# Optimization experiments

Hardware: AMD Instinct MI355X
Metric: run time of the kernel (lower is better)

The kernel has to match this reference:

```python
import jax, jax.numpy as jnp
import numpy as np

NUM_ATOMS = 100000
NUM_BONDS = 200000
MAX_NB = 6
ATOM_FDIM = 133
BOND_FDIM = 147
HIDDEN = 300
READOUT = 512
DEPTH = 6
ATOMS_PER_MOL = 25
NUM_MOLS = NUM_ATOMS // ATOMS_PER_MOL


def setup_inputs() -> dict:
    key = jax.random.key(0)
    ks = jax.random.split(key, 16)
    s = 0.02
    inp = {
        "f_atoms": jax.random.normal(ks[0], (NUM_ATOMS, ATOM_FDIM), jnp.float32),
        "f_bonds": jax.random.normal(ks[1], (NUM_BONDS, BOND_FDIM), jnp.float32),
        "a2b": jax.random.randint(ks[2], (NUM_ATOMS, MAX_NB), 0, NUM_BONDS),
        "b2a": jax.random.randint(ks[3], (NUM_BONDS,), 0, NUM_ATOMS),
        "b2revb": jax.random.randint(ks[4], (NUM_BONDS,), 0, NUM_BONDS),
        "mol_id": jnp.arange(NUM_ATOMS) // ATOMS_PER_MOL,
        # parameters (Linear: y = x @ W + b)
        "W_i": jax.random.normal(ks[5], (BOND_FDIM, HIDDEN), jnp.float32) * s,
        "b_i": jnp.zeros((HIDDEN,), jnp.float32),
        "W_h": jax.random.normal(ks[6], (HIDDEN, HIDDEN), jnp.float32) * s,
        "b_h": jnp.zeros((HIDDEN,), jnp.float32),
        "W_o": jax.random.normal(ks[7], (ATOM_FDIM + HIDDEN, HIDDEN), jnp.float32) * s,
        "b_o": jnp.zeros((HIDDEN,), jnp.float32),
        "W_fc0": jax.random.normal(ks[8], (HIDDEN, READOUT), jnp.float32) * s,
        "b_fc0": jnp.zeros((READOUT,), jnp.float32),
        "W_fc1": jax.random.normal(ks[9], (READOUT, READOUT), jnp.float32) * s,
        "b_fc1": jnp.zeros((READOUT,), jnp.float32),
        "W_last": jax.random.normal(ks[10], (READOUT, 1), jnp.float32) * s,
        "b_last": jnp.zeros((1,), jnp.float32),
    }
    return inp


def reference(f_atoms, f_bonds, W_i, b_i, W_h, b_h, W_o, b_o,
              W_fc0, b_fc0, W_fc1, b_fc1, W_last, b_last,
              a2b, b2a, b2revb, mol_id):
    relu = jax.nn.relu
    # input = W_i(f_bonds); message = relu(input)  (dropout p=0 -> identity)
    inp = f_bonds @ W_i + b_i                      # [B, H]
    message = relu(inp)
    for _ in range(DEPTH - 1):
        nei = message[a2b]                          # [A, nb, H] gather
        a_message = nei.sum(axis=1)                 # [A, H]
        rev_message = message[b2revb]               # [B, H]
        message = a_message[b2a] - rev_message      # [B, H]
        message = relu(inp + (message @ W_h + b_h))
    # final atom aggregation
    a_message = message[a2b].sum(axis=1)            # [A, H]
    a_input = jnp.concatenate([f_atoms, a_message], axis=1)
    atom_hiddens = relu(a_input @ W_o + b_o)        # [A, H]
    # molecule mean-pool (a_scope -> segment mean over mol_id)
    sums = jax.ops.segment_sum(atom_hiddens, mol_id, num_segments=NUM_MOLS)
    counts = jax.ops.segment_sum(jnp.ones((atom_hiddens.shape[0], 1), atom_hiddens.dtype),
                                 mol_id, num_segments=NUM_MOLS)
    mol_vecs = sums / jnp.maximum(counts, 1.0)      # [M, H]
    # readout MLP
    h = relu(mol_vecs @ W_fc0 + b_fc0)
    h = relu(h @ W_fc1 + b_fc1)
    out = h @ W_last + b_last                       # [M, 1]
    return out.reshape(-1)
```

## Files before the change

### kernel.cpp

```cpp
#include <hip/hip_runtime.h>

#define NATOMS 100000
#define NBONDS 200000
#define NMOLS  4000

typedef __bf16 bf16x8 __attribute__((ext_vector_type(8)));
typedef float  f32x4  __attribute__((ext_vector_type(4)));

__device__ unsigned short g_packWi [5  * 40 * 512];
__device__ unsigned short g_packWh [10 * 40 * 512];
__device__ unsigned short g_packWoT[5  * 40 * 512];
__device__ unsigned short g_packWoB[10 * 40 * 512];

__device__ __forceinline__ float bf2f(unsigned short u) {
    union { unsigned int i; float f; } c; c.i = ((unsigned int)u) << 16; return c.f;
}
__device__ __forceinline__ unsigned short f2bf(float f) {
    union { float f; unsigned int i; } c; c.f = f;
    unsigned int r = (c.i + 0x7FFFu + ((c.i >> 16) & 1u)) >> 16;
    return (unsigned short)r;
}
__device__ __forceinline__ unsigned int relu2(unsigned int u) {
    if (u & 0x00008000u) u &= 0xFFFF0000u;
    if (u & 0x80000000u) u &= 0x0000FFFFu;
    return u;
}

__global__ void pack_weights(const float* __restrict__ W_i,
                             const float* __restrict__ W_h,
                             const float* __restrict__ W_o)
{
    const int gid = blockIdx.x * blockDim.x + threadIdx.x;
    if (gid >= 1200 * 512) return;
    const int gg = gid >> 9;
    const int t  = gid & 511;
    const float* src; int K; unsigned short* dst; int lg;
    if (gg < 200)      { lg = gg;       src = W_i;             K = 147; dst = g_packWi; }
    else if (gg < 600) { lg = gg - 200; src = W_h;             K = 300; dst = g_packWh; }
    else if (gg < 800) { lg = gg - 600; src = W_o;             K = 133; dst = g_packWoT; }
    else               { lg = gg - 800; src = W_o + 133 * 300; K = 300; dst = g_packWoB; }
    const int s  = lg / 40, r = lg % 40;
    const int nh = r / 20, fr = (r % 20) >> 1, hl = r & 1;
    const int ln = t >> 3, j = t & 7;
    const int k = 32 * s + 8 * (ln >> 4) + j;
    const int n = 16 * (nh * 10 + fr) + (ln & 15);
    float val = (k < K && n < 300) ? src[k * 300 + n] : 0.f;
    unsigned short hi = f2bf(val);
    dst[(long)lg * 512 + t] = hl ? f2bf(val - bf2f(hi)) : hi;
}

__global__ __launch_bounds__(512, 4)
void gemm_mfma5(const void* __restrict__ Ap, int a16, int sel,
                const float* __restrict__ bias, const float* __restrict__ Cin,
                void* __restrict__ outR, int r16,
                unsigned short* __restrict__ outP16,
                long M, int K, int ksteps, int do_relu)
{
    __shared__ unsigned long long lds8[57344 / 8];
    unsigned short* Asm0 = (unsigned short*)lds8;
    unsigned short* Bsm  = (unsigned short*)lds8 + 8192;
    unsigned short* ep   = (unsigned short*)lds8;

    const unsigned short* pp =
        (sel == 0) ? g_packWi : (sel == 1) ? g_packWh :
        (sel == 2) ? g_packWoT : g_packWoB;

    const int tid = threadIdx.x;
    const int wv  = tid >> 6;
    const int ln  = tid & 63;
    const int l15 = ln & 15;
    const int g   = ln >> 4;
    const int wm  = wv >> 1;
    const int wn  = wv & 1;
    const long row0 = (long)blockIdx.x * 128;

    f32x4 acc[2][10];
#pragma unroll
    for (int m = 0; m < 2; ++m)
#pragma unroll
        for (int f = 0; f < 10; ++f) acc[m][f] = (f32x4){0.f, 0.f, 0.f, 0.f};

    int aoff[2];
#pragma unroll
    for (int m = 0; m < 2; ++m) {
        const int r = wm * 32 + m * 16 + l15;
        aoff[m] = r * 32 + 8 * (g ^ ((r >> 1) & 3));
    }

    const int srow = tid >> 2, sq = tid & 3;
    const int sqs  = sq ^ ((srow >> 1) & 3);

#define STAGE_A(BUF, SS)                                                       \
    do {                                                                       \
        if (a16) {                                                             \
            const char* src = (const char*)Ap +                                \
                (row0 + srow) * (size_t)600 + (SS) * 64 + sqs * 16;            \
            char* dst = (char*)Asm0 + (BUF) * 8192 + srow * 64 + sq * 16;      \
            __builtin_amdgcn_global_load_lds(                                  \
                (const __attribute__((address_space(1))) void*)src,            \
                (__attribute__((address_space(3))) void*)dst, 16, 0, 0);       \
        } else {                                                               \
            const float* A = (const float*)Ap;                                 \
            const long gr = row0 + srow;                                       \
            const int kb = (SS) * 32 + sqs * 8;                                \
            unsigned short tv[8];                                              \
            _Pragma("unroll")                                                  \
            for (int e = 0; e < 8; ++e)                                        \
                tv[e] = (gr < M && kb + e < K) ? f2bf(A[gr * (long)K + kb + e]) \
                                               : (unsigned short)0;            \
            ushort4 w0 = {tv[0], tv[1], tv[2], tv[3]};                         \
            ushort4 w1 = {tv[4], tv[5], tv[6], tv[7]};                         \
            *(ushort4*)(Asm0 + (BUF) * 4096 + srow * 32 + sq * 8)     = w0;    \
            *(ushort4*)(Asm0 + (BUF) * 4096 + srow * 32 + sq * 8 + 4) = w1;    \
        }                                                                      \
    } while (0)

#define STAGE_B(SS)                                                            \
    do {                                                                       \
        _Pragma("unroll")                                                      \
        for (int i = 0; i < 5; ++i) {                                          \
            const char* src = (const char*)pp + (size_t)(SS) * 40960           \
                              + i * 8192 + tid * 16;                           \
            char* dst = (char*)Bsm + i * 8192 + tid * 16;                      \
            __builtin_amdgcn_global_load_lds(                                  \
                (const __attribute__((address_space(1))) void*)src,            \
                (__attribute__((address_space(3))) void*)dst, 16, 0, 0);       \
        }                                                                      \
    } while (0)

    STAGE_A(0, 0);
    for (int s = 0; s < ksteps; ++s) {
        STAGE_B(s);
        if (s + 1 < ksteps) STAGE_A((s + 1) & 1, s + 1);
        __syncthreads();
        const unsigned short* Ab = Asm0 + (s & 1) * 4096;
        bf16x8 av[2];
#pragma unroll
        for (int m = 0; m < 2; ++m) av[m] = *(const bf16x8*)(Ab + aoff[m]);
#pragma unroll
        for (int f = 0; f < 10; ++f) {
            const int ch = wn * 20 + f * 2;
            bf16x8 bh = *(const bf16x8*)(Bsm + (ch + 0) * 512 + ln * 8);
            bf16x8 bl = *(const bf16x8*)(Bsm + (ch + 1) * 512 + ln * 8);
#pragma unroll
            for (int m = 0; m < 2; ++m) {
                acc[m][f] = __builtin_amdgcn_mfma_f32_16x16x32_bf16(av[m], bh, acc[m][f], 0, 0, 0);
                acc[m][f] = __builtin_amdgcn_mfma_f32_16x16x32_bf16(av[m], bl, acc[m][f], 0, 0, 0);
            }
        }
        __syncthreads();
    }
#undef STAGE_A
#undef STAGE_B

    if (r16) {
        for (int p = 0; p < 2; ++p) {
            if (p) __syncthreads();
            if ((wm >> 1) == p) {
                const int rbase = (wm & 1) * 32;
#pragma unroll
                for (int f = 0; f < 10; ++f) {
                    const int n = (wn * 10 + f) * 16 + l15;
                    if (n >= 300) continue;
                    const float bv = bias ? bias[n] : 0.f;
#pragma unroll
                    for (int m = 0; m < 2; ++m)
#pragma unroll
                        for (int rr = 0; rr < 4; ++rr) {
                            const int rl = rbase + m * 16 + g * 4 + rr;
                            ep[rl * 304 + n] = f2bf(acc[m][f][rr] + bv);
                        }
                }
            }
            __syncthreads();
            for (int c = tid; c < 4800; c += 512) {
                const int row = c / 75, off = c - row * 75;
                const long grow = row0 + p * 64 + row;
                if (grow >= M) continue;
                uint2 v = *(const uint2*)(ep + row * 304 + off * 4);
                if (outP16)
                    *(uint2*)(outP16 + grow * 300 + off * 4) = v;
                if (do_relu) { v.x = relu2(v.x); v.y = relu2(v.y); }
                *(uint2*)((unsigned short*)outR + grow * 300 + off * 4) = v;
            }
        }
    } else {
#pragma unroll
        for (int f = 0; f < 10; ++f) {
            const int n = (wn * 10 + f) * 16 + l15;
            if (n >= 300) continue;
            const float bv = bias ? bias[n] : 0.f;
#pragma unroll
            for (int m = 0; m < 2; ++m) {
#pragma unroll
                for (int rr = 0; rr < 4; ++rr) {
                    const long row = row0 + wm * 32 + m * 16 + g * 4 + rr;
                    if (row >= M) continue;
                    float v = acc[m][f][rr] + bv;
                    if (Cin) v += Cin[row * 300 + n];
                    if (do_relu) v = fmaxf(v, 0.f);
                    ((float*)outR)[row * 300 + n] = v;
                }
            }
        }
    }
}

__global__ __launch_bounds__(256)
void gemm_flex(const float* __restrict__ A,
               const float* __restrict__ W,
               const float* __restrict__ bias,
               float* __restrict__ outR,
               int M, int K, int N, int do_relu)
{
    __shared__ float As[16][132];
    __shared__ float Bs[16][132];

    const int tid  = threadIdx.x;
    const int tx   = tid & 15;
    const int ty   = tid >> 4;
    const int row0 = blockIdx.y * 128;
    const int col0 = blockIdx.x * 128;

    float acc[8][8];
#pragma unroll
    for (int i = 0; i < 8; ++i)
#pragma unroll
        for (int j = 0; j < 8; ++j) acc[i][j] = 0.f;

    for (int k0 = 0; k0 < K; k0 += 16) {
        {
            const int c  = tid & 15;
            const int rb = tid >> 4;
#pragma unroll
            for (int i = 0; i < 8; ++i) {
                const int r  = rb + (i << 4);
                const int gr = row0 + r, gc = k0 + c;
                As[c][r] = (gr < M && gc < K) ? A[(long)gr * K + gc] : 0.f;
            }
        }
        {
            const int c  = tid & 127;
            const int rb = tid >> 7;
#pragma unroll
            for (int i = 0; i < 8; ++i) {
                const int r  = rb + (i << 1);
                const int gr = k0 + r, gc = col0 + c;
                Bs[r][c] = (gr < K && gc < N) ? W[(long)gr * N + gc] : 0.f;
            }
        }
        __syncthreads();
#pragma unroll
        for (int kk = 0; kk < 16; ++kk) {
            const float4* As4 = reinterpret_cast<const float4*>(&As[kk][0]);
            const float4* Bs4 = reinterpret_cast<const float4*>(&Bs[kk][0]);
            float4 a0 = As4[ty], a1 = As4[ty + 16];
            float4 b0 = Bs4[tx], b1 = Bs4[tx + 16];
            float av[8] = {a0.x, a0.y, a0.z, a0.w, a1.x, a1.y, a1.z, a1.w};
            float bv[8] = {b0.x, b0.y, b0.z, b0.w, b1.x, b1.y, b1.z, b1.w};
#pragma unroll
            for (int i = 0; i < 8; ++i)
#pragma unroll
                for (int j = 0; j < 8; ++j)
                    acc[i][j] = fmaf(av[i], bv[j], acc[i][j]);
        }
        __syncthreads();
    }
#pragma unroll
    for (int i = 0; i < 8; ++i) {
        const int lr = (i < 4) ? (ty * 4 + i) : (64 + ty * 4 + (i - 4));
        const int gr = row0 + lr;
        if (gr >= M) continue;
#pragma unroll
        for (int j = 0; j < 8; ++j) {
            const int lc = (j < 4) ? (tx * 4 + j) : (64 + tx * 4 + (j - 4));
            const int gc = col0 + lc;
            if (gc >= N) continue;
            float v = acc[i][j];
            if (bias) v += bias[gc];
            if (do_relu) v = fmaxf(v, 0.f);
            outR[(long)gr * N + gc] = v;
        }
    }
}

__global__ void aggregate_bf16(const unsigned short* __restrict__ src,
                               const int* __restrict__ a2b,
                               unsigned short* __restrict__ dst)
{
    const int idx = blockIdx.x * blockDim.x + threadIdx.x;
    if (idx >= NATOMS * 75) return;
    const int a = idx / 75;
    const int q = idx - a * 75;
    const int* nb = a2b + a * 6;
    float s0 = 0.f, s1 = 0.f, s2 = 0.f, s3 = 0.f;
#pragma unroll
    for (int k = 0; k < 6; ++k) {
        const ushort4 v = *reinterpret_cast<const ushort4*>(src + (long)nb[k] * 300 + (q << 2));
        s0 += bf2f(v.x); s1 += bf2f(v.y); s2 += bf2f(v.z); s3 += bf2f(v.w);
    }
    ushort4 r;
    r.x = f2bf(s0); r.y = f2bf(s1); r.z = f2bf(s2); r.w = f2bf(s3);
    *reinterpret_cast<ushort4*>(dst + ((long)idx << 2)) = r;
}

__global__ void fused_update(const unsigned short* __restrict__ t,
                             const int* __restrict__ a2b,
                             const int* __restrict__ b2a,
                             const int* __restrict__ b2revb,
                             const float* __restrict__ b_h,
                             const unsigned short* __restrict__ inp,
                             unsigned short* __restrict__ dst)
{
    const int idx = blockIdx.x * blockDim.x + threadIdx.x;
    if (idx >= NBONDS * 75) return;
    const int b = idx / 75;
    const int q = idx - b * 75;
    const long own = (long)b * 300 + (q << 2);
    const ushort4 vi = *reinterpret_cast<const ushort4*>(inp + own);
    const float4 vh = *reinterpret_cast<const float4*>(b_h + (q << 2));
    float s0 = bf2f(vi.x) + vh.x;
    float s1 = bf2f(vi.y) + vh.y;
    float s2 = bf2f(vi.z) + vh.z;
    float s3 = bf2f(vi.w) + vh.w;
    const int a = b2a[b];
    const int* nb = a2b + a * 6;
#pragma unroll
    for (int k = 0; k < 6; ++k) {
        const ushort4 v = *reinterpret_cast<const ushort4*>(t + (long)nb[k] * 300 + (q << 2));
        s0 += bf2f(v.x); s1 += bf2f(v.y); s2 += bf2f(v.z); s3 += bf2f(v.w);
    }
    {
        const ushort4 v = *reinterpret_cast<const ushort4*>(t + (long)b2revb[b] * 300 + (q << 2));
        s0 -= bf2f(v.x); s1 -= bf2f(v.y); s2 -= bf2f(v.z); s3 -= bf2f(v.w);
    }
    ushort4 o;
    o.x = f2bf(fmaxf(s0, 0.f));
    o.y = f2bf(fmaxf(s1, 0.f));
    o.z = f2bf(fmaxf(s2, 0.f));
    o.w = f2bf(fmaxf(s3, 0.f));
    *reinterpret_cast<ushort4*>(dst + own) = o;
}

__global__ void pool_kernel(const float* __restrict__ ah, float* __restrict__ mol)
{
    const int idx = blockIdx.x * blockDim.x + threadIdx.x;
    if (idx >= NMOLS * 75) return;
    const int m = idx / 75;
    const int q = idx - m * 75;
    const float* base = ah + (long)m * 25 * 300 + (q << 2);
    float s0 = 0.f, s1 = 0.f, s2 = 0.f, s3 = 0.f;
#pragma unroll
    for (int a = 0; a < 25; ++a) {
        const float4 v = *reinterpret_cast<const float4*>(base + a * 300);
        s0 += v.x; s1 += v.y; s2 += v.z; s3 += v.w;
    }
    float4 r; r.x = s0 / 25.f; r.y = s1 / 25.f; r.z = s2 / 25.f; r.w = s3 / 25.f;
    *reinterpret_cast<float4*>(mol + ((long)idx << 2)) = r;
}

__global__ void diag_kernel(float* __restrict__ out, float wsmb)
{
    const int i = blockIdx.x * blockDim.x + threadIdx.x;
    if (i < NMOLS) out[i] = (i == 0) ? wsmb : 0.f;
}

extern "C" void kernel_launch(void* const* d_in, const int* in_sizes, int n_in,
                              void* d_out, int out_size, void* d_ws, size_t ws_size,
                              hipStream_t stream)
{
    const float* f_atoms = (const float*)d_in[0];
    const float* f_bonds = (const float*)d_in[1];
    const int*   a2b     = (const int*)d_in[2];
    const int*   b2a     = (const int*)d_in[3];
    const int*   b2revb  = (const int*)d_in[4];
    const float* W_i    = (const float*)d_in[6];
    const float* b_i    = (const float*)d_in[7];
    const float* W_h    = (const float*)d_in[8];
    const float* b_h    = (const float*)d_in[9];
    const float* W_o    = (const float*)d_in[10];
    const float* b_o    = (const float*)d_in[11];
    const float* W_fc0  = (const float*)d_in[12];
    const float* b_fc0  = (const float*)d_in[13];
    const float* W_fc1  = (const float*)d_in[14];
    const float* b_fc1  = (const float*)d_in[15];
    const float* W_last = (const float*)d_in[16];
    const float* b_last = (const float*)d_in[17];
    float* out = (float*)d_out;

    if (ws_size < 240000000ull) {
        diag_kernel<<<(NMOLS + 255) / 256, 256, 0, stream>>>(out, (float)(ws_size >> 20));
        return;
    }

    const int gBond = (NBONDS + 127) / 128;
    const int gAtom = (NATOMS + 127) / 128;
    const int aggBlocks = (NATOMS * 75 + 255) / 256;
    const int updBlocks = (NBONDS * 75 + 255) / 256;

    pack_weights<<<(1200 * 512 + 255) / 256, 256, 0, stream>>>(W_i, W_h, W_o);

    if (ws_size >= 360000000ull) {
        unsigned short* inpB = (unsigned short*)d_ws;
        unsigned short* msgB = (unsigned short*)((char*)d_ws + 120000000);
        unsigned short* tB   = (unsigned short*)((char*)d_ws + 240000000);
        unsigned short* amB  = (unsigned short*)d_ws;
        float* tmpF = (float*)((char*)d_ws + 120000000);
        float* molF = (float*)((char*)d_ws + 240000000);
        float* h0   = molF + 2000000;
        float* h1   = molF + 5000000;

        gemm_mfma5<<<gBond, 512, 0, stream>>>(f_bonds, 0, 0, b_i, nullptr,
                                              msgB, 1, inpB, NBONDS, 147, 5, 1);
        for (int d = 0; d < 5; ++d) {
            gemm_mfma5<<<gBond, 512, 0, stream>>>(msgB, 1, 1, nullptr, nullptr,
                                                  tB, 1, nullptr, NBONDS, 300, 10, 0);
            fused_update<<<updBlocks, 256, 0, stream>>>(tB, a2b, b2a, b2revb, b_h,
                                                        inpB, msgB);
        }
        aggregate_bf16<<<aggBlocks, 256, 0, stream>>>(msgB, a2b, amB);
        gemm_mfma5<<<gAtom, 512, 0, stream>>>(f_atoms, 0, 2, nullptr, nullptr,
                                              tmpF, 0, nullptr, NATOMS, 133, 5, 0);
        gemm_mfma5<<<gAtom, 512, 0, stream>>>(amB, 1, 3, b_o, tmpF,
                                              tmpF, 0, nullptr, NATOMS, 300, 10, 1);
        pool_kernel<<<(NMOLS * 75 + 255) / 256, 256, 0, stream>>>(tmpF, molF);
        gemm_flex<<<dim3(4, 32), 256, 0, stream>>>(molF, W_fc0, b_fc0, h0, NMOLS, 300, 512, 1);
        gemm_flex<<<dim3(4, 32), 256, 0, stream>>>(h0, W_fc1, b_fc1, h1, NMOLS, 512, 512, 1);
        gemm_flex<<<dim3(1, 32), 256, 0, stream>>>(h1, W_last, b_last, out, NMOLS, 512, 1, 0);
    } else {
        unsigned short* msgB = (unsigned short*)d_ws;
        unsigned short* tB   = (unsigned short*)((char*)d_ws + 120000000);
        unsigned short* amB  = tB;
        float* tmpF = (float*)d_ws;
        float* molF = (float*)((char*)d_ws + 180000000);
        float* h0   = molF + 2000000;
        float* h1   = molF + 5000000;

        gemm_mfma5<<<gBond, 512, 0, stream>>>(f_bonds, 0, 0, b_i, nullptr,
                                              msgB, 1, nullptr, NBONDS, 147, 5, 1);
        for (int d = 0; d < 5; ++d) {
            gemm_mfma5<<<gBond, 512, 0, stream>>>(msgB, 1, 1, nullptr, nullptr,
                                                  tB, 1, nullptr, NBONDS, 300, 10, 0);
            gemm_mfma5<<<gBond, 512, 0, stream>>>(f_bonds, 0, 0, b_i, nullptr,
                                                  msgB, 1, nullptr, NBONDS, 147, 5, 0);
            fused_update<<<updBlocks, 256, 0, stream>>>(tB, a2b, b2a, b2revb, b_h,
                                                        msgB, msgB);
        }
        aggregate_bf16<<<aggBlocks, 256, 0, stream>>>(msgB, a2b, amB);
        gemm_mfma5<<<gAtom, 512, 0, stream>>>(f_atoms, 0, 2, nullptr, nullptr,
                                              tmpF, 0, nullptr, NATOMS, 133, 5, 0);
        gemm_mfma5<<<gAtom, 512, 0, stream>>>(amB, 1, 3, b_o, tmpF,
                                              tmpF, 0, nullptr, NATOMS, 300, 10, 1);
        pool_kernel<<<(NMOLS * 75 + 255) / 256, 256, 0, stream>>>(tmpF, molF);
        gemm_flex<<<dim3(4, 32), 256, 0, stream>>>(molF, W_fc0, b_fc0, h0, NMOLS, 300, 512, 1);
        gemm_flex<<<dim3(4, 32), 256, 0, stream>>>(h0, W_fc1, b_fc1, h1, NMOLS, 512, 512, 1);
        gemm_flex<<<dim3(1, 32), 256, 0, stream>>>(h1, W_last, b_last, out, NMOLS, 512, 1, 0);
    }
}
```

Baseline: 2.317 ms.

## Double-buffer B weight tiles and remap waves to 2x4 grid in MFMA GEMM

The GEMM kernel now double-buffers the packed weight (B) tiles in LDS alongside A, so the next k-step's A and B loads are issued before computing the current one, leaving one barrier per step instead of two. The wave layout changes from 4x2 to 2x4, with each wave covering 64 rows by 5 column fragments, which raises A-fragment reuse per B load. The weight packing is simplified to a linear fragment order to match. LDS use grows to 96KB per block, which may limit blocks per CU and lower occupancy.

```diff
diff --git a/kernel.cpp b/kernel.cpp
--- a/kernel.cpp
+++ b/kernel.cpp
@@ -39,27 +39,27 @@
     else if (gg < 600) { lg = gg - 200; src = W_h;             K = 300; dst = g_packWh; }
     else if (gg < 800) { lg = gg - 600; src = W_o;             K = 133; dst = g_packWoT; }
     else               { lg = gg - 800; src = W_o + 133 * 300; K = 300; dst = g_packWoB; }
-    const int s  = lg / 40, r = lg % 40;
-    const int nh = r / 20, fr = (r % 20) >> 1, hl = r & 1;
+    const int s = lg / 40, r = lg % 40;
+    const int f = r >> 1, hl = r & 1;
     const int ln = t >> 3, j = t & 7;
     const int k = 32 * s + 8 * (ln >> 4) + j;
-    const int n = 16 * (nh * 10 + fr) + (ln & 15);
+    const int n = 16 * f + (ln & 15);
     float val = (k < K && n < 300) ? src[k * 300 + n] : 0.f;
     unsigned short hi = f2bf(val);
     dst[(long)lg * 512 + t] = hl ? f2bf(val - bf2f(hi)) : hi;
 }
 
-__global__ __launch_bounds__(512, 4)
-void gemm_mfma5(const void* __restrict__ Ap, int a16, int sel,
+__global__ __launch_bounds__(512)
+void gemm_mfma6(const void* __restrict__ Ap, int a16, int sel,
                 const float* __restrict__ bias, const float* __restrict__ Cin,
                 void* __restrict__ outR, int r16,
                 unsigned short* __restrict__ outP16,
                 long M, int K, int ksteps, int do_relu)
 {
-    __shared__ unsigned long long lds8[57344 / 8];
-    unsigned short* Asm0 = (unsigned short*)lds8;
-    unsigned short* Bsm  = (unsigned short*)lds8 + 8192;
-    unsigned short* ep   = (unsigned short*)lds8;
+    __shared__ unsigned long long lds8[98304 / 8];
+    unsigned short* Asm = (unsigned short*)lds8;
+    unsigned short* Bsm = (unsigned short*)lds8 + 8192;
+    unsigned short* ep  = (unsigned short*)lds8;
 
     const unsigned short* pp =
         (sel == 0) ? g_packWi : (sel == 1) ? g_packWh :
@@ -70,20 +70,20 @@
     const int ln  = tid & 63;
     const int l15 = ln & 15;
     const int g   = ln >> 4;
-    const int wm  = wv >> 1;
-    const int wn  = wv & 1;
+    const int wm  = wv >> 2;
+    const int wn  = wv & 3;
     const long row0 = (long)blockIdx.x * 128;
 
-    f32x4 acc[2][10];
-#pragma unroll
-    for (int m = 0; m < 2; ++m)
-#pragma unroll
-        for (int f = 0; f < 10; ++f) acc[m][f] = (f32x4){0.f, 0.f, 0.f, 0.f};
-
-    int aoff[2];
-#pragma unroll
-    for (int m = 0; m < 2; ++m) {
-        const int r = wm * 32 + m * 16 + l15;
+    f32x4 acc[4][5];
+#pragma unroll
+    for (int m = 0; m < 4; ++m)
+#pragma unroll
+        for (int f = 0; f < 5; ++f) acc[m][f] = (f32x4){0.f, 0.f, 0.f, 0.f};
+
+    int aoff[4];
+#pragma unroll
+    for (int m = 0; m < 4; ++m) {
+        const int r = wm * 64 + m * 16 + l15;
         aoff[m] = r * 32 + 8 * (g ^ ((r >> 1) & 3));
     }
 
@@ -95,7 +95,7 @@
         if (a16) {                                                             \
             const char* src = (const char*)Ap +                                \
                 (row0 + srow) * (size_t)600 + (SS) * 64 + sqs * 16;            \
-            char* dst = (char*)Asm0 + (BUF) * 8192 + srow * 64 + sq * 16;      \
+            char* dst = (char*)Asm + (BUF) * 8192 + srow * 64 + sq * 16;       \
             __builtin_amdgcn_global_load_lds(                                  \
                 (const __attribute__((address_space(1))) void*)src,            \
                 (__attribute__((address_space(3))) void*)dst, 16, 0, 0);       \
@@ -110,18 +110,18 @@
                                                : (unsigned short)0;            \
             ushort4 w0 = {tv[0], tv[1], tv[2], tv[3]};                         \
             ushort4 w1 = {tv[4], tv[5], tv[6], tv[7]};                         \
-            *(ushort4*)(Asm0 + (BUF) * 4096 + srow * 32 + sq * 8)     = w0;    \
-            *(ushort4*)(Asm0 + (BUF) * 4096 + srow * 32 + sq * 8 + 4) = w1;    \
+            *(ushort4*)(Asm + (BUF) * 4096 + srow * 32 + sq * 8)     = w0;     \
+            *(ushort4*)(Asm + (BUF) * 4096 + srow * 32 + sq * 8 + 4) = w1;     \
         }                                                                      \
     } while (0)
 
-#define STAGE_B(SS)                                                            \
+#define STAGE_B(BUF, SS)                                                       \
     do {                                                                       \
         _Pragma("unroll")                                                      \
         for (int i = 0; i < 5; ++i) {                                          \
             const char* src = (const char*)pp + (size_t)(SS) * 40960           \
                               + i * 8192 + tid * 16;                           \
-            char* dst = (char*)Bsm + i * 8192 + tid * 16;                      \
+            char* dst = (char*)Bsm + (BUF) * 40960 + i * 8192 + tid * 16;      \
             __builtin_amdgcn_global_load_lds(                                  \
                 (const __attribute__((address_space(1))) void*)src,            \
                 (__attribute__((address_space(3))) void*)dst, 16, 0, 0);       \
@@ -129,24 +129,30 @@
     } while (0)
 
     STAGE_A(0, 0);
+    STAGE_B(0, 0);
+    __syncthreads();
     for (int s = 0; s < ksteps; ++s) {
-        STAGE_B(s);
-        if (s + 1 < ksteps) STAGE_A((s + 1) & 1, s + 1);
-        __syncthreads();
-        const unsigned short* Ab = Asm0 + (s & 1) * 4096;
-        bf16x8 av[2];
-#pragma unroll
-        for (int m = 0; m < 2; ++m) av[m] = *(const bf16x8*)(Ab + aoff[m]);
-#pragma unroll
-        for (int f = 0; f < 10; ++f) {
-            const int ch = wn * 20 + f * 2;
-            bf16x8 bh = *(const bf16x8*)(Bsm + (ch + 0) * 512 + ln * 8);
-            bf16x8 bl = *(const bf16x8*)(Bsm + (ch + 1) * 512 + ln * 8);
-#pragma unroll
-            for (int m = 0; m < 2; ++m) {
+        const int cur = s & 1;
+        if (s + 1 < ksteps) {
+            STAGE_A(cur ^ 1, s + 1);
+            STAGE_B(cur ^ 1, s + 1);
+        }
+        const unsigned short* Ab = Asm + cur * 4096;
+        const unsigned short* Bb = Bsm + cur * 20480;
+        bf16x8 av[4];
+#pragma unroll
+        for (int m = 0; m < 4; ++m) av[m] = *(const bf16x8*)(Ab + aoff[m]);
+#pragma unroll
+        for (int f = 0; f < 5; ++f) {
+            const int fg = wn * 5 + f;
+            bf16x8 bh = *(const bf16x8*)(Bb + (2 * fg + 0) * 512 + ln * 8);
+            bf16x8 bl = *(const bf16x8*)(Bb + (2 * fg + 1) * 512 + ln * 8);
+#pragma unroll
+            for (int m = 0; m < 4; ++m)
                 acc[m][f] = __builtin_amdgcn_mfma_f32_16x16x32_bf16(av[m], bh, acc[m][f], 0, 0, 0);
+#pragma unroll
+            for (int m = 0; m < 4; ++m)
                 acc[m][f] = __builtin_amdgcn_mfma_f32_16x16x32_bf16(av[m], bl, acc[m][f], 0, 0, 0);
-            }
         }
         __syncthreads();
     }
@@ -156,18 +162,17 @@
     if (r16) {
         for (int p = 0; p < 2; ++p) {
             if (p) __syncthreads();
-            if ((wm >> 1) == p) {
-                const int rbase = (wm & 1) * 32;
-#pragma unroll
-                for (int f = 0; f < 10; ++f) {
-                    const int n = (wn * 10 + f) * 16 + l15;
+            if (wm == p) {
+#pragma unroll
+                for (int f = 0; f < 5; ++f) {
+                    const int n = (wn * 5 + f) * 16 + l15;
                     if (n >= 300) continue;
                     const float bv = bias ? bias[n] : 0.f;
 #pragma unroll
-                    for (int m = 0; m < 2; ++m)
+                    for (int m = 0; m < 4; ++m)
 #pragma unroll
                         for (int rr = 0; rr < 4; ++rr) {
-                            const int rl = rbase + m * 16 + g * 4 + rr;
+                            const int rl = m * 16 + g * 4 + rr;
                             ep[rl * 304 + n] = f2bf(acc[m][f][rr] + bv);
                         }
                 }
@@ -186,15 +191,15 @@
         }
     } else {
 #pragma unroll
-        for (int f = 0; f < 10; ++f) {
-            const int n = (wn * 10 + f) * 16 + l15;
+        for (int f = 0; f < 5; ++f) {
+            const int n = (wn * 5 + f) * 16 + l15;
             if (n >= 300) continue;
             const float bv = bias ? bias[n] : 0.f;
 #pragma unroll
-            for (int m = 0; m < 2; ++m) {
+            for (int m = 0; m < 4; ++m) {
 #pragma unroll
                 for (int rr = 0; rr < 4; ++rr) {
-                    const long row = row0 + wm * 32 + m * 16 + g * 4 + rr;
+                    const long row = row0 + wm * 64 + m * 16 + g * 4 + rr;
                     if (row >= M) continue;
                     float v = acc[m][f][rr] + bv;
                     if (Cin) v += Cin[row * 300 + n];
@@ -410,18 +415,18 @@
         float* h0   = molF + 2000000;
         float* h1   = molF + 5000000;
 
-        gemm_mfma5<<<gBond, 512, 0, stream>>>(f_bonds, 0, 0, b_i, nullptr,
+        gemm_mfma6<<<gBond, 512, 0, stream>>>(f_bonds, 0, 0, b_i, nullptr,
                                               msgB, 1, inpB, NBONDS, 147, 5, 1);
         for (int d = 0; d < 5; ++d) {
-            gemm_mfma5<<<gBond, 512, 0, stream>>>(msgB, 1, 1, nullptr, nullptr,
+            gemm_mfma6<<<gBond, 512, 0, stream>>>(msgB, 1, 1, nullptr, nullptr,
                                                   tB, 1, nullptr, NBONDS, 300, 10, 0);
             fused_update<<<updBlocks, 256, 0, stream>>>(tB, a2b, b2a, b2revb, b_h,
                                                         inpB, msgB);
         }
         aggregate_bf16<<<aggBlocks, 256, 0, stream>>>(msgB, a2b, amB);
-        gemm_mfma5<<<gAtom, 512, 0, stream>>>(f_atoms, 0, 2, nullptr, nullptr,
+        gemm_mfma6<<<gAtom, 512, 0, stream>>>(f_atoms, 0, 2, nullptr, nullptr,
                                               tmpF, 0, nullptr, NATOMS, 133, 5, 0);
-        gemm_mfma5<<<gAtom, 512, 0, stream>>>(amB, 1, 3, b_o, tmpF,
+        gemm_mfma6<<<gAtom, 512, 0, stream>>>(amB, 1, 3, b_o, tmpF,
                                               tmpF, 0, nullptr, NATOMS, 300, 10, 1);
         pool_kernel<<<(NMOLS * 75 + 255) / 256, 256, 0, stream>>>(tmpF, molF);
         gemm_flex<<<dim3(4, 32), 256, 0, stream>>>(molF, W_fc0, b_fc0, h0, NMOLS, 300, 512, 1);
@@ -436,20 +441,20 @@
         float* h0   = molF + 2000000;
         float* h1   = molF + 5000000;
 
-        gemm_mfma5<<<gBond, 512, 0, stream>>>(f_bonds, 0, 0, b_i, nullptr,
+        gemm_mfma6<<<gBond, 512, 0, stream>>>(f_bonds, 0, 0, b_i, nullptr,
                                               msgB, 1, nullptr, NBONDS, 147, 5, 1);
         for (int d = 0; d < 5; ++d) {
-            gemm_mfma5<<<gBond, 512, 0, stream>>>(msgB, 1, 1, nullptr, nullptr,
+            gemm_mfma6<<<gBond, 512, 0, stream>>>(msgB, 1, 1, nullptr, nullptr,
                                                   tB, 1, nullptr, NBONDS, 300, 10, 0);
-            gemm_mfma5<<<gBond, 512, 0, stream>>>(f_bonds, 0, 0, b_i, nullptr,
+            gemm_mfma6<<<gBond, 512, 0, stream>>>(f_bonds, 0, 0, b_i, nullptr,
                                                   msgB, 1, nullptr, NBONDS, 147, 5, 0);
             fused_update<<<updBlocks, 256, 0, stream>>>(tB, a2b, b2a, b2revb, b_h,
                                                         msgB, msgB);
         }
         aggregate_bf16<<<aggBlocks, 256, 0, stream>>>(msgB, a2b, amB);
-        gemm_mfma5<<<gAtom, 512, 0, stream>>>(f_atoms, 0, 2, nullptr, nullptr,
+        gemm_mfma6<<<gAtom, 512, 0, stream>>>(f_atoms, 0, 2, nullptr, nullptr,
                                               tmpF, 0, nullptr, NATOMS, 133, 5, 0);
-        gemm_mfma5<<<gAtom, 512, 0, stream>>>(amB, 1, 3, b_o, tmpF,
+        gemm_mfma6<<<gAtom, 512, 0, stream>>>(amB, 1, 3, b_o, tmpF,
                                               tmpF, 0, nullptr, NATOMS, 300, 10, 1);
         pool_kernel<<<(NMOLS * 75 + 255) / 256, 256, 0, stream>>>(tmpF, molF);
         gemm_flex<<<dim3(4, 32), 256, 0, stream>>>(molF, W_fc0, b_fc0, h0, NMOLS, 300, 512, 1);
```

Result: slower. 2.537 ms (+9.5%).

## Fuse message gather into W_h GEMM A-loading and fuse update epilogue

Applied to the files above, without the earlier changes.

The message-passing step now gathers the neighbour messages (six a2b neighbours of the source atom minus the reverse bond) inside the GEMM's A-tile staging, and applies the input residual, bias and ReLU in the GEMM epilogue. This removes the separate fused_update kernel and the intermediate tB round-trip per depth, and uses ping-pong message buffers. Weight packing is simplified to a linear column-fragment order. In exchange, the GEMM A-staging becomes seven scattered row loads per tile and per k-step instead of asynchronous direct-to-LDS loads. The per-bond gather is also recomputed for every k-step, and the recomputed sum is rounded to bf16 before the matmul.

```diff
diff --git a/kernel.cpp b/kernel.cpp
--- a/kernel.cpp
+++ b/kernel.cpp
@@ -39,27 +39,32 @@
     else if (gg < 600) { lg = gg - 200; src = W_h;             K = 300; dst = g_packWh; }
     else if (gg < 800) { lg = gg - 600; src = W_o;             K = 133; dst = g_packWoT; }
     else               { lg = gg - 800; src = W_o + 133 * 300; K = 300; dst = g_packWoB; }
-    const int s  = lg / 40, r = lg % 40;
-    const int nh = r / 20, fr = (r % 20) >> 1, hl = r & 1;
+    const int s = lg / 40, r = lg % 40;
+    const int f = r >> 1, hl = r & 1;
     const int ln = t >> 3, j = t & 7;
     const int k = 32 * s + 8 * (ln >> 4) + j;
-    const int n = 16 * (nh * 10 + fr) + (ln & 15);
+    const int n = 16 * f + (ln & 15);
     float val = (k < K && n < 300) ? src[k * 300 + n] : 0.f;
     unsigned short hi = f2bf(val);
     dst[(long)lg * 512 + t] = hl ? f2bf(val - bf2f(hi)) : hi;
 }
 
 __global__ __launch_bounds__(512, 4)
-void gemm_mfma5(const void* __restrict__ Ap, int a16, int sel,
-                const float* __restrict__ bias, const float* __restrict__ Cin,
+void gemm_mfma8(const void* __restrict__ Ap, int mode, int sel,
+                const float* __restrict__ bias,
+                const float* __restrict__ cinF,
+                const unsigned short* __restrict__ cin16,
                 void* __restrict__ outR, int r16,
                 unsigned short* __restrict__ outP16,
+                const int* __restrict__ b2a,
+                const int* __restrict__ a2b,
+                const int* __restrict__ b2revb,
                 long M, int K, int ksteps, int do_relu)
 {
     __shared__ unsigned long long lds8[57344 / 8];
-    unsigned short* Asm0 = (unsigned short*)lds8;
-    unsigned short* Bsm  = (unsigned short*)lds8 + 8192;
-    unsigned short* ep   = (unsigned short*)lds8;
+    unsigned short* Asm = (unsigned short*)lds8;
+    unsigned short* Bsm = (unsigned short*)lds8 + 8192;
+    unsigned short* ep  = (unsigned short*)lds8;
 
     const unsigned short* pp =
         (sel == 0) ? g_packWi : (sel == 1) ? g_packWh :
@@ -90,15 +95,56 @@
     const int srow = tid >> 2, sq = tid & 3;
     const int sqs  = sq ^ ((srow >> 1) & 3);
 
+    int gnb0 = 0, gnb1 = 0, gnb2 = 0, gnb3 = 0, gnb4 = 0, gnb5 = 0, grev = 0;
+    bool gok = false;
+    if (mode == 2) {
+        const long brow = row0 + srow;
+        gok = (brow < M);
+        const int bi = gok ? (int)brow : 0;
+        const int a  = b2a[bi];
+        grev = b2revb[bi];
+        const int* nb = a2b + a * 6;
+        gnb0 = nb[0]; gnb1 = nb[1]; gnb2 = nb[2];
+        gnb3 = nb[3]; gnb4 = nb[4]; gnb5 = nb[5];
+    }
+
+#define GROW(idx, sgn)                                                         \
+    do {                                                                       \
+        const unsigned short* rp = (const unsigned short*)Ap +                 \
+            (long)(idx) * 300 + kb;                                            \
+        const uint2 u0 = *(const uint2*)(rp);                                  \
+        const uint2 u1 = *(const uint2*)(rp + 4);                              \
+        s0 sgn bf2f((unsigned short)(u0.x & 0xFFFF));                          \
+        s1 sgn bf2f((unsigned short)(u0.x >> 16));                             \
+        s2 sgn bf2f((unsigned short)(u0.y & 0xFFFF));                          \
+        s3 sgn bf2f((unsigned short)(u0.y >> 16));                             \
+        s4 sgn bf2f((unsigned short)(u1.x & 0xFFFF));                          \
+        s5 sgn bf2f((unsigned short)(u1.x >> 16));                             \
+        s6 sgn bf2f((unsigned short)(u1.y & 0xFFFF));                          \
+        s7 sgn bf2f((unsigned short)(u1.y >> 16));                             \
+    } while (0)
+
 #define STAGE_A(BUF, SS)                                                       \
     do {                                                                       \
-        if (a16) {                                                             \
+        if (mode == 1) {                                                       \
             const char* src = (const char*)Ap +                                \
                 (row0 + srow) * (size_t)600 + (SS) * 64 + sqs * 16;            \
-            char* dst = (char*)Asm0 + (BUF) * 8192 + srow * 64 + sq * 16;      \
+            char* dst = (char*)Asm + (BUF) * 8192 + srow * 64 + sq * 16;       \
             __builtin_amdgcn_global_load_lds(                                  \
                 (const __attribute__((address_space(1))) void*)src,            \
                 (__attribute__((address_space(3))) void*)dst, 16, 0, 0);       \
+        } else if (mode == 2) {                                                \
+            float s0=0.f,s1=0.f,s2=0.f,s3=0.f,s4=0.f,s5=0.f,s6=0.f,s7=0.f;     \
+            const int kb = (SS) * 32 + sqs * 8;                                \
+            if (gok) {                                                         \
+                GROW(gnb0, +=); GROW(gnb1, +=); GROW(gnb2, +=);                \
+                GROW(gnb3, +=); GROW(gnb4, +=); GROW(gnb5, +=);                \
+                GROW(grev, -=);                                                \
+            }                                                                  \
+            ushort4 w0 = {f2bf(s0), f2bf(s1), f2bf(s2), f2bf(s3)};             \
+            ushort4 w1 = {f2bf(s4), f2bf(s5), f2bf(s6), f2bf(s7)};             \
+            *(ushort4*)(Asm + (BUF) * 4096 + srow * 32 + sq * 8)     = w0;     \
+            *(ushort4*)(Asm + (BUF) * 4096 + srow * 32 + sq * 8 + 4) = w1;     \
         } else {                                                               \
             const float* A = (const float*)Ap;                                 \
             const long gr = row0 + srow;                                       \
@@ -110,8 +156,8 @@
                                                : (unsigned short)0;            \
             ushort4 w0 = {tv[0], tv[1], tv[2], tv[3]};                         \
             ushort4 w1 = {tv[4], tv[5], tv[6], tv[7]};                         \
-            *(ushort4*)(Asm0 + (BUF) * 4096 + srow * 32 + sq * 8)     = w0;    \
-            *(ushort4*)(Asm0 + (BUF) * 4096 + srow * 32 + sq * 8 + 4) = w1;    \
+            *(ushort4*)(Asm + (BUF) * 4096 + srow * 32 + sq * 8)     = w0;     \
+            *(ushort4*)(Asm + (BUF) * 4096 + srow * 32 + sq * 8 + 4) = w1;     \
         }                                                                      \
     } while (0)
 
@@ -133,7 +179,7 @@
         STAGE_B(s);
         if (s + 1 < ksteps) STAGE_A((s + 1) & 1, s + 1);
         __syncthreads();
-        const unsigned short* Ab = Asm0 + (s & 1) * 4096;
+        const unsigned short* Ab = Asm + (s & 1) * 4096;
         bf16x8 av[2];
 #pragma unroll
         for (int m = 0; m < 2; ++m) av[m] = *(const bf16x8*)(Ab + aoff[m]);
@@ -152,6 +198,7 @@
     }
 #undef STAGE_A
 #undef STAGE_B
+#undef GROW
 
     if (r16) {
         for (int p = 0; p < 2; ++p) {
@@ -178,10 +225,24 @@
                 const long grow = row0 + p * 64 + row;
                 if (grow >= M) continue;
                 uint2 v = *(const uint2*)(ep + row * 304 + off * 4);
-                if (outP16)
-                    *(uint2*)(outP16 + grow * 300 + off * 4) = v;
-                if (do_relu) { v.x = relu2(v.x); v.y = relu2(v.y); }
-                *(uint2*)((unsigned short*)outR + grow * 300 + off * 4) = v;
+                const long gbase = grow * 300 + off * 4;
+                if (outP16) *(uint2*)(outP16 + gbase) = v;
+                if (cin16) {
+                    const uint2 iv = *(const uint2*)(cin16 + gbase);
+                    float f0 = bf2f((unsigned short)(v.x & 0xFFFF)) + bf2f((unsigned short)(iv.x & 0xFFFF));
+                    float f1 = bf2f((unsigned short)(v.x >> 16))    + bf2f((unsigned short)(iv.x >> 16));
+                    float f2 = bf2f((unsigned short)(v.y & 0xFFFF)) + bf2f((unsigned short)(iv.y & 0xFFFF));
+                    float f3 = bf2f((unsigned short)(v.y >> 16))    + bf2f((unsigned short)(iv.y >> 16));
+                    if (do_relu) {
+                        f0 = fmaxf(f0, 0.f); f1 = fmaxf(f1, 0.f);
+                        f2 = fmaxf(f2, 0.f); f3 = fmaxf(f3, 0.f);
+                    }
+                    v.x = (unsigned int)f2bf(f0) | ((unsigned int)f2bf(f1) << 16);
+                    v.y = (unsigned int)f2bf(f2) | ((unsigned int)f2bf(f3) << 16);
+                } else if (do_relu) {
+                    v.x = relu2(v.x); v.y = relu2(v.y);
+                }
+                *(uint2*)((unsigned short*)outR + gbase) = v;
             }
         }
     } else {
@@ -197,7 +258,7 @@
                     const long row = row0 + wm * 32 + m * 16 + g * 4 + rr;
                     if (row >= M) continue;
                     float v = acc[m][f][rr] + bv;
-                    if (Cin) v += Cin[row * 300 + n];
+                    if (cinF) v += cinF[row * 300 + n];
                     if (do_relu) v = fmaxf(v, 0.f);
                     ((float*)outR)[row * 300 + n] = v;
                 }
@@ -402,27 +463,40 @@
 
     if (ws_size >= 360000000ull) {
         unsigned short* inpB = (unsigned short*)d_ws;
-        unsigned short* msgB = (unsigned short*)((char*)d_ws + 120000000);
-        unsigned short* tB   = (unsigned short*)((char*)d_ws + 240000000);
-        unsigned short* amB  = (unsigned short*)d_ws;
-        float* tmpF = (float*)((char*)d_ws + 120000000);
-        float* molF = (float*)((char*)d_ws + 240000000);
-        float* h0   = molF + 2000000;
-        float* h1   = molF + 5000000;
-
-        gemm_mfma5<<<gBond, 512, 0, stream>>>(f_bonds, 0, 0, b_i, nullptr,
-                                              msgB, 1, inpB, NBONDS, 147, 5, 1);
+        unsigned short* bufA = (unsigned short*)((char*)d_ws + 120000000);
+        unsigned short* bufB = (unsigned short*)((char*)d_ws + 240000000);
+        unsigned short* amB  = inpB;
+        float* molF = nullptr;
+        gemm_mfma8<<<gBond, 512, 0, stream>>>(f_bonds, 0, 0, b_i,
+                                              nullptr, nullptr,
+                                              bufA, 1, inpB,
+                                              nullptr, nullptr, nullptr,
+                                              NBONDS, 147, 5, 1);
+        unsigned short* cur = bufA;
+        unsigned short* oth = bufB;
         for (int d = 0; d < 5; ++d) {
-            gemm_mfma5<<<gBond, 512, 0, stream>>>(msgB, 1, 1, nullptr, nullptr,
-                                                  tB, 1, nullptr, NBONDS, 300, 10, 0);
-            fused_update<<<updBlocks, 256, 0, stream>>>(tB, a2b, b2a, b2revb, b_h,
-                                                        inpB, msgB);
-        }
-        aggregate_bf16<<<aggBlocks, 256, 0, stream>>>(msgB, a2b, amB);
-        gemm_mfma5<<<gAtom, 512, 0, stream>>>(f_atoms, 0, 2, nullptr, nullptr,
-                                              tmpF, 0, nullptr, NATOMS, 133, 5, 0);
-        gemm_mfma5<<<gAtom, 512, 0, stream>>>(amB, 1, 3, b_o, tmpF,
-                                              tmpF, 0, nullptr, NATOMS, 300, 10, 1);
+            gemm_mfma8<<<gBond, 512, 0, stream>>>(cur, 2, 1, b_h,
+                                                  nullptr, inpB,
+                                                  oth, 1, nullptr,
+                                                  b2a, a2b, b2revb,
+                                                  NBONDS, 300, 10, 1);
+            unsigned short* tmp = cur; cur = oth; oth = tmp;
+        }
+        aggregate_bf16<<<aggBlocks, 256, 0, stream>>>(cur, a2b, amB);
+        float* tmpF = (float*)oth;
+        gemm_mfma8<<<gAtom, 512, 0, stream>>>(f_atoms, 0, 2, nullptr,
+                                              nullptr, nullptr,
+                                              tmpF, 0, nullptr,
+                                              nullptr, nullptr, nullptr,
+                                              NATOMS, 133, 5, 0);
+        gemm_mfma8<<<gAtom, 512, 0, stream>>>(amB, 1, 3, b_o,
+                                              tmpF, nullptr,
+                                              tmpF, 0, nullptr,
+                                              nullptr, nullptr, nullptr,
+                                              NATOMS, 300, 10, 1);
+        molF = (float*)cur;
+        float* h0 = molF + 2000000;
+        float* h1 = molF + 5000000;
         pool_kernel<<<(NMOLS * 75 + 255) / 256, 256, 0, stream>>>(tmpF, molF);
         gemm_flex<<<dim3(4, 32), 256, 0, stream>>>(molF, W_fc0, b_fc0, h0, NMOLS, 300, 512, 1);
         gemm_flex<<<dim3(4, 32), 256, 0, stream>>>(h0, W_fc1, b_fc1, h1, NMOLS, 512, 512, 1);
@@ -436,21 +510,36 @@
         float* h0   = molF + 2000000;
         float* h1   = molF + 5000000;
 
-        gemm_mfma5<<<gBond, 512, 0, stream>>>(f_bonds, 0, 0, b_i, nullptr,
-                                              msgB, 1, nullptr, NBONDS, 147, 5, 1);
+        gemm_mfma8<<<gBond, 512, 0, stream>>>(f_bonds, 0, 0, b_i,
+                                              nullptr, nullptr,
+                                              msgB, 1, nullptr,
+                                              nullptr, nullptr, nullptr,
+                                              NBONDS, 147, 5, 1);
         for (int d = 0; d < 5; ++d) {
-            gemm_mfma5<<<gBond, 512, 0, stream>>>(msgB, 1, 1, nullptr, nullptr,
-                                                  tB, 1, nullptr, NBONDS, 300, 10, 0);
-            gemm_mfma5<<<gBond, 512, 0, stream>>>(f_bonds, 0, 0, b_i, nullptr,
-                                                  msgB, 1, nullptr, NBONDS, 147, 5, 0);
+            gemm_mfma8<<<gBond, 512, 0, stream>>>(msgB, 1, 1, nullptr,
+                                                  nullptr, nullptr,
+                                                  tB, 1, nullptr,
+                                                  nullptr, nullptr, nullptr,
+                                                  NBONDS, 300, 10, 0);
+            gemm_mfma8<<<gBond, 512, 0, stream>>>(f_bonds, 0, 0, b_i,
+                                                  nullptr, nullptr,
+                                                  msgB, 1, nullptr,
+                                                  nullptr, nullptr, nullptr,
+                                                  NBONDS, 147, 5, 0);
             fused_update<<<updBlocks, 256, 0, stream>>>(tB, a2b, b2a, b2revb, b_h,
                                                         msgB, msgB);
         }
         aggregate_bf16<<<aggBlocks, 256, 0, stream>>>(msgB, a2b, amB);
-        gemm_mfma5<<<gAtom, 512, 0, stream>>>(f_atoms, 0, 2, nullptr, nullptr,
-                                              tmpF, 0, nullptr, NATOMS, 133, 5, 0);
-        gemm_mfma5<<<gAtom, 512, 0, stream>>>(amB, 1, 3, b_o, tmpF,
-                                              tmpF, 0, nullptr, NATOMS, 300, 10, 1);
+        gemm_mfma8<<<gAtom, 512, 0, stream>>>(f_atoms, 0, 2, nullptr,
+                                              nullptr, nullptr,
+                                              tmpF, 0, nullptr,
+                                              nullptr, nullptr, nullptr,
+                                              NATOMS, 133, 5, 0);
+        gemm_mfma8<<<gAtom, 512, 0, stream>>>(amB, 1, 3, b_o,
+                                              tmpF, nullptr,
+                                              tmpF, 0, nullptr,
+                                              nullptr, nullptr, nullptr,
+                                              NATOMS, 300, 10, 1);
         pool_kernel<<<(NMOLS * 75 + 255) / 256, 256, 0, stream>>>(tmpF, molF);
         gemm_flex<<<dim3(4, 32), 256, 0, stream>>>(molF, W_fc0, b_fc0, h0, NMOLS, 300, 512, 1);
         gemm_flex<<<dim3(4, 32), 256, 0, stream>>>(h0, W_fc1, b_fc1, h1, NMOLS, 512, 512, 1);
```

Measured after the change: 4.601 ms. 98.6% more time.
